# Performance work log

Measured on AMD Instinct MI355X. Metric: run time of the kernel, lower is better.

The kernel has to match this reference:

```python
import jax, jax.numpy as jnp
import numpy as np

B, N, G = 8, 262144, 64
EPS = 1e-6


def _log_transform(x):
    return jnp.sign(x) * jnp.log1p(jnp.abs(x))


def _group_mean_depth(points, valid, groups):
    # points: (B,N,3), valid: (B,N) bool, groups: (B,N) int in [0,G)
    z = points[..., 2]
    w = valid.astype(z.dtype)
    seg = (groups.astype(jnp.int32) + jnp.arange(B, dtype=jnp.int32)[:, None] * G).ravel()
    sums = jax.ops.segment_sum((z * w).ravel(), seg, num_segments=B * G)
    cnts = jax.ops.segment_sum(w.ravel(), seg, num_segments=B * G)
    mean = jnp.where(cnts > 0, sums / jnp.maximum(cnts, 1.0), 1.0)  # empty group -> 1.0 (skipped in torch loop)
    safe = jnp.maximum(jnp.abs(mean), EPS)
    per_point = safe[seg].reshape(z.shape)
    return jnp.where(valid, per_point, 1.0)


def _normalize_points(points, valid, groups):
    md = _group_mean_depth(points, valid, groups)
    return jnp.where(valid[..., None], points, 0.0) / md[..., None]


def _masked_mean(loss, valid):
    vm = valid if loss.ndim == valid.ndim else jnp.broadcast_to(valid[..., None], loss.shape)
    return jnp.where(vm, loss, 0.0).sum() / (vm.sum().astype(loss.dtype) + 1e-6)


def setup_inputs() -> dict:
    key = jax.random.key(0)
    ks = jax.random.split(key, 13)
    f = lambda k, s: jax.random.normal(k, s, dtype=jnp.float32)
    return {
        'pred_points': f(ks[0], (B, N, 3)),
        'target_points': f(ks[1], (B, N, 3)),
        'pred_2d': f(ks[2], (B, N, 2)),
        'target_2d': f(ks[3], (B, N, 2)),
        'pred_vis': f(ks[4], (B, N, 1)),
        'target_vis': jax.random.uniform(ks[5], (B, N), dtype=jnp.float32),
        'pred_disp': f(ks[6], (B, N, 3)),
        'target_disp': f(ks[7], (B, N, 3)),
        'pred_normal': f(ks[8], (B, N, 3)),
        'target_normal': f(ks[9], (B, N, 3)),
        'confidence': f(ks[10], (B, N, 1)),
        'mask': jax.random.randint(ks[11], (B, N), 0, 2, dtype=jnp.int32),
        'groups': jax.random.randint(ks[12], (B, N), 0, G, dtype=jnp.int32),
    }


def reference(pred_points, target_points, pred_2d, target_2d, pred_vis, target_vis,
              pred_disp, target_disp, pred_normal, target_normal, confidence, mask, groups):
    lambda_3d, lambda_raw_3d, lambda_2d = 1.0, 0.0, 0.1
    lambda_vis, lambda_disp, lambda_normal, lambda_conf = 0.1, 0.1, 0.5, 0.2
    valid = mask.astype(bool)

    # L_3D: per-group scale-invariant normalization + log transform + masked L1
    pn = _log_transform(_normalize_points(pred_points, valid, groups))
    tn = _log_transform(_normalize_points(target_points, valid, groups))
    l_3d = _masked_mean(jnp.abs(pn - tn), valid)

    # L_raw3D: raw camera-space L1 (weight 0 by default)
    l_raw3d = _masked_mean(jnp.abs(pred_points - target_points), valid)

    # L_2D
    l_2d = _masked_mean(jnp.abs(pred_2d - target_2d), valid)

    # L_vis: BCE with logits
    x = pred_vis[..., 0]
    bce = jnp.maximum(x, 0.0) - x * target_vis + jnp.log1p(jnp.exp(-jnp.abs(x)))
    l_vis = _masked_mean(bce, valid)

    # L_disp
    l_disp = _masked_mean(jnp.abs(pred_disp - target_disp), valid)

    # L_normal: 1 - cosine similarity of unit-normalized vectors
    def _unit(v):
        n = jnp.linalg.norm(v, axis=-1, keepdims=True)
        return v / jnp.maximum(n, 1e-12)
    cos = (_unit(pred_normal) * _unit(target_normal)).sum(-1)
    l_normal = _masked_mean(1.0 - cos, valid)

    # L_conf: Kendall penalty s = -log(c)
    l_conf = _masked_mean(confidence[..., 0], valid)

    return (lambda_3d * l_3d + lambda_raw_3d * l_raw3d + lambda_2d * l_2d
            + lambda_vis * l_vis + lambda_disp * l_disp
            + lambda_normal * l_normal + lambda_conf * l_conf)
```

## Files before the change

kernel.cpp:

```cpp
#include <hip/hip_runtime.h>
#include <math.h>

#define GG   64
#define NBG  512
#define TOT  2097152
#define PTS  1024
#define NBLK (TOT / PTS)

#define ZP_F   0
#define ZT_F   512
#define CNT_F  1024
#define PAIR_F 1536
#define NV_F   2560
#define PART_F 2816
#define WS_ZERO_BYTES (1536 * 4)

#define LN2   0.6931471805599453f
#define LOG2E 1.4426950408889634f

typedef float vf4 __attribute__((ext_vector_type(4)));
typedef int   vi4 __attribute__((ext_vector_type(4)));

__device__ __forceinline__ float fexp2(float x) { return __builtin_amdgcn_exp2f(x); }
__device__ __forceinline__ float flog2(float x) { return __builtin_amdgcn_logf(x); }
__device__ __forceinline__ float flog1p(float x) { return flog2(1.0f + x) * LN2; }

__device__ __forceinline__ float4 ntl4(const float4* p) {
    vf4 v = __builtin_nontemporal_load((const vf4*)p);
    return make_float4(v.x, v.y, v.z, v.w);
}
__device__ __forceinline__ int4 ntl4i(const int4* p) {
    vi4 v = __builtin_nontemporal_load((const vi4*)p);
    return make_int4(v.x, v.y, v.z, v.w);
}

__device__ __forceinline__ float wredf(float v) {
#pragma unroll
    for (int o = 32; o > 0; o >>= 1) v += __shfl_down(v, o, 64);
    return v;
}

__global__ __launch_bounds__(256) void k_group(const float* __restrict__ pp,
                                               const float* __restrict__ tp,
                                               const int* __restrict__ mask,
                                               const int* __restrict__ grp,
                                               float* __restrict__ ws) {
    __shared__ float4 bufA[768], bufB[768];
    __shared__ float sP[GG], sT[GG], sC[GG];
    const int tid = threadIdx.x;
    if (tid < GG) { sP[tid] = 0.f; sT[tid] = 0.f; sC[tid] = 0.f; }

    const int base = blockIdx.x * PTS;
    const int b = base >> 18;
    const int p0 = base + 4 * tid;

    const float4* gx = (const float4*)(pp + (size_t)base * 3);
    const float4* gy = (const float4*)(tp + (size_t)base * 3);
#pragma unroll
    for (int j = 0; j < 3; j++) {
        bufA[tid + 256 * j] = ntl4(&gx[tid + 256 * j]);
        bufB[tid + 256 * j] = ntl4(&gy[tid + 256 * j]);
    }
    const int4 M  = ntl4i((const int4*)(mask + p0));
    const int4 Gp = ntl4i((const int4*)(grp + p0));
    __syncthreads();

    float4 a0 = bufA[3 * tid], a1 = bufA[3 * tid + 1], a2 = bufA[3 * tid + 2];
    float4 b0 = bufB[3 * tid], b1 = bufB[3 * tid + 1], b2 = bufB[3 * tid + 2];
    if (M.x) { atomicAdd(&sP[Gp.x], a0.z); atomicAdd(&sT[Gp.x], b0.z); atomicAdd(&sC[Gp.x], 1.f); }
    if (M.y) { atomicAdd(&sP[Gp.y], a1.y); atomicAdd(&sT[Gp.y], b1.y); atomicAdd(&sC[Gp.y], 1.f); }
    if (M.z) { atomicAdd(&sP[Gp.z], a2.x); atomicAdd(&sT[Gp.z], b2.x); atomicAdd(&sC[Gp.z], 1.f); }
    if (M.w) { atomicAdd(&sP[Gp.w], a2.w); atomicAdd(&sT[Gp.w], b2.w); atomicAdd(&sC[Gp.w], 1.f); }
    __syncthreads();

    if (tid < GG) {
        float c = sC[tid];
        if (c != 0.0f) {
            int e = b * GG + tid;
            atomicAdd(&ws[ZP_F + e], sP[tid]);
            atomicAdd(&ws[ZT_F + e], sT[tid]);
            atomicAdd(&ws[CNT_F + e], c);
        }
    }
}

__global__ __launch_bounds__(512) void k_groups_final(float* __restrict__ ws) {
    __shared__ float red[NBG];
    int j = threadIdx.x;
    float c  = ws[CNT_F + j];
    float mP = (c > 0.f) ? (ws[ZP_F + j] / fmaxf(c, 1.f)) : 1.0f;
    float mT = (c > 0.f) ? (ws[ZT_F + j] / fmaxf(c, 1.f)) : 1.0f;
    ws[PAIR_F + 2 * j]     = 1.0f / fmaxf(fabsf(mP), 1e-6f);
    ws[PAIR_F + 2 * j + 1] = 1.0f / fmaxf(fabsf(mT), 1e-6f);
    red[j] = c;
    __syncthreads();
    for (int s = 256; s > 0; s >>= 1) {
        if (j < s) red[j] += red[j + s];
        __syncthreads();
    }
    if (j == 0) ws[NV_F] = red[0];
}

__global__ __launch_bounds__(256) void k_loss(const float* __restrict__ pp,
                                              const float* __restrict__ tp,
                                              const float* __restrict__ p2,
                                              const float* __restrict__ t2,
                                              const float* __restrict__ pv,
                                              const float* __restrict__ tv,
                                              const float* __restrict__ pd,
                                              const float* __restrict__ td,
                                              const float* __restrict__ pn,
                                              const float* __restrict__ tn,
                                              const float* __restrict__ cf,
                                              const int* __restrict__ mask,
                                              const int* __restrict__ grp,
                                              float* __restrict__ ws) {
    __shared__ float4 bufA[768], bufB[768];
    const int tid = threadIdx.x;
    const int base = blockIdx.x * PTS;
    const int p0 = base + 4 * tid;
    const int bb6 = (base >> 18) << 6;
    const float* pairs = ws + PAIR_F;

    const int4 M  = ntl4i((const int4*)(mask + p0));
    const int4 Gp = ntl4i((const int4*)(grp + p0));
    const float w[4] = {(float)M.x, (float)M.y, (float)M.z, (float)M.w};
    const int Gs[4] = {Gp.x, Gp.y, Gp.z, Gp.w};
    float iP[4], iT[4];
#pragma unroll
    for (int k = 0; k < 4; k++) {
        float2 pr = *(const float2*)(pairs + 2 * (bb6 | Gs[k]));
        iP[k] = pr.x; iT[k] = pr.y;
    }

    float s3d = 0.f, s2 = 0.f, sv = 0.f, sd = 0.f, sn = 0.f, sc = 0.f;

    {
        float4 Aa = ntl4(((const float4*)(p2 + 2 * (size_t)p0)) + 0);
        float4 Ab = ntl4(((const float4*)(p2 + 2 * (size_t)p0)) + 1);
        float4 Ba = ntl4(((const float4*)(t2 + 2 * (size_t)p0)) + 0);
        float4 Bb = ntl4(((const float4*)(t2 + 2 * (size_t)p0)) + 1);
        s2 = w[0] * (fabsf(Aa.x - Ba.x) + fabsf(Aa.y - Ba.y))
           + w[1] * (fabsf(Aa.z - Ba.z) + fabsf(Aa.w - Ba.w))
           + w[2] * (fabsf(Ab.x - Bb.x) + fabsf(Ab.y - Bb.y))
           + w[3] * (fabsf(Ab.z - Bb.z) + fabsf(Ab.w - Bb.w));
    }
    {
        float4 X  = ntl4((const float4*)(pv + p0));
        float4 Tg = ntl4((const float4*)(tv + p0));
        float4 C  = ntl4((const float4*)(cf + p0));
        const float xs[4] = {X.x, X.y, X.z, X.w};
        const float ts[4] = {Tg.x, Tg.y, Tg.z, Tg.w};
        const float cs[4] = {C.x, C.y, C.z, C.w};
#pragma unroll
        for (int k = 0; k < 4; k++) {
            float x = xs[k];
            float soft = flog2(1.0f + fexp2(-fabsf(x) * LOG2E)) * LN2;
            sv += w[k] * (fmaxf(x, 0.f) - x * ts[k] + soft);
            sc += w[k] * cs[k];
        }
    }

    {
        const float4* gx = (const float4*)(pp + (size_t)base * 3);
        const float4* gy = (const float4*)(tp + (size_t)base * 3);
#pragma unroll
        for (int j = 0; j < 3; j++) {
            bufA[tid + 256 * j] = ntl4(&gx[tid + 256 * j]);
            bufB[tid + 256 * j] = ntl4(&gy[tid + 256 * j]);
        }
        __syncthreads();
        float P[12], T[12];
        *(float4*)&P[0] = bufA[3 * tid]; *(float4*)&P[4] = bufA[3 * tid + 1]; *(float4*)&P[8] = bufA[3 * tid + 2];
        *(float4*)&T[0] = bufB[3 * tid]; *(float4*)&T[4] = bufB[3 * tid + 1]; *(float4*)&T[8] = bufB[3 * tid + 2];
        __syncthreads();
#pragma unroll
        for (int k = 0; k < 4; k++) {
            float acc = 0.f;
#pragma unroll
            for (int c = 0; c < 3; c++) {
                float a = P[3 * k + c] * iP[k];
                float b = T[3 * k + c] * iT[k];
                acc += fabsf(copysignf(flog1p(fabsf(a)), a) - copysignf(flog1p(fabsf(b)), b));
            }
            s3d += w[k] * acc;
        }
    }
    {
        const float4* gx = (const float4*)(pd + (size_t)base * 3);
        const float4* gy = (const float4*)(td + (size_t)base * 3);
#pragma unroll
        for (int j = 0; j < 3; j++) {
            bufA[tid + 256 * j] = ntl4(&gx[tid + 256 * j]);
            bufB[tid + 256 * j] = ntl4(&gy[tid + 256 * j]);
        }
        __syncthreads();
        float P[12], T[12];
        *(float4*)&P[0] = bufA[3 * tid]; *(float4*)&P[4] = bufA[3 * tid + 1]; *(float4*)&P[8] = bufA[3 * tid + 2];
        *(float4*)&T[0] = bufB[3 * tid]; *(float4*)&T[4] = bufB[3 * tid + 1]; *(float4*)&T[8] = bufB[3 * tid + 2];
        __syncthreads();
#pragma unroll
        for (int k = 0; k < 4; k++) {
            float acc = fabsf(P[3 * k] - T[3 * k]) + fabsf(P[3 * k + 1] - T[3 * k + 1])
                      + fabsf(P[3 * k + 2] - T[3 * k + 2]);
            sd += w[k] * acc;
        }
    }
    {
        const float4* gx = (const float4*)(pn + (size_t)base * 3);
        const float4* gy = (const float4*)(tn + (size_t)base * 3);
#pragma unroll
        for (int j = 0; j < 3; j++) {
            bufA[tid + 256 * j] = ntl4(&gx[tid + 256 * j]);
            bufB[tid + 256 * j] = ntl4(&gy[tid + 256 * j]);
        }
        __syncthreads();
        float P[12], T[12];
        *(float4*)&P[0] = bufA[3 * tid]; *(float4*)&P[4] = bufA[3 * tid + 1]; *(float4*)&P[8] = bufA[3 * tid + 2];
        *(float4*)&T[0] = bufB[3 * tid]; *(float4*)&T[4] = bufB[3 * tid + 1]; *(float4*)&T[8] = bufB[3 * tid + 2];
#pragma unroll
        for (int k = 0; k < 4; k++) {
            float ax = P[3 * k], ay = P[3 * k + 1], az = P[3 * k + 2];
            float bx = T[3 * k], by = T[3 * k + 1], bz = T[3 * k + 2];
            float na = fmaf(ax, ax, fmaf(ay, ay, az * az));
            float nb = fmaf(bx, bx, fmaf(by, by, bz * bz));
            float dot = fmaf(ax, bx, fmaf(ay, by, az * bz));
            float r = __frsqrt_rn(fmaxf(na, 1e-24f)) * __frsqrt_rn(fmaxf(nb, 1e-24f));
            sn += w[k] * (1.0f - dot * r);
        }
    }

    __shared__ float sred[4][6];
    float vals[6] = {s3d, s2, sv, sd, sn, sc};
    int wid = threadIdx.x >> 6, lane = threadIdx.x & 63;
#pragma unroll
    for (int k = 0; k < 6; k++) {
        float r = wredf(vals[k]);
        if (lane == 0) sred[wid][k] = r;
    }
    __syncthreads();
    if (threadIdx.x < 6) {
        float tt = sred[0][threadIdx.x] + sred[1][threadIdx.x]
                 + sred[2][threadIdx.x] + sred[3][threadIdx.x];
        ws[PART_F + threadIdx.x * NBLK + blockIdx.x] = tt;
    }
}

__global__ __launch_bounds__(256) void k_final(const float* __restrict__ ws,
                                               float* __restrict__ out) {
    const float* part = ws + PART_F;
    double loc[6] = {0, 0, 0, 0, 0, 0};
    for (int j = threadIdx.x; j < NBLK; j += 256) {
#pragma unroll
        for (int k = 0; k < 6; k++) loc[k] += (double)part[k * NBLK + j];
    }
    __shared__ double dred[4][6];
    int wid = threadIdx.x >> 6, lane = threadIdx.x & 63;
#pragma unroll
    for (int k = 0; k < 6; k++) {
        double v = loc[k];
#pragma unroll
        for (int o = 32; o > 0; o >>= 1) v += __shfl_down(v, o, 64);
        if (lane == 0) dred[wid][k] = v;
    }
    __syncthreads();
    if (threadIdx.x == 0) {
        double a[6];
#pragma unroll
        for (int k = 0; k < 6; k++)
            a[k] = dred[0][k] + dred[1][k] + dred[2][k] + dred[3][k];
        double nv = (double)ws[NV_F];
        double d1 = nv + 1e-6;
        double d3 = 3.0 * nv + 1e-6;
        double l3d   = a[0] / d3;
        double l2d   = a[1] / (2.0 * nv + 1e-6);
        double lvis  = a[2] / d1;
        double ldisp = a[3] / d3;
        double lnorm = a[4] / d1;
        double lconf = a[5] / d1;
        out[0] = (float)(l3d + 0.1 * (l2d + lvis + ldisp) + 0.5 * lnorm + 0.2 * lconf);
    }
}

extern "C" void kernel_launch(void* const* d_in, const int* in_sizes, int n_in,
                              void* d_out, int out_size, void* d_ws, size_t ws_size,
                              hipStream_t stream) {
    const float* pp = (const float*)d_in[0];
    const float* tp = (const float*)d_in[1];
    const float* p2 = (const float*)d_in[2];
    const float* t2 = (const float*)d_in[3];
    const float* pv = (const float*)d_in[4];
    const float* tv = (const float*)d_in[5];
    const float* pd = (const float*)d_in[6];
    const float* td = (const float*)d_in[7];
    const float* pn = (const float*)d_in[8];
    const float* tn = (const float*)d_in[9];
    const float* cf = (const float*)d_in[10];
    const int* mask = (const int*)d_in[11];
    const int* grp  = (const int*)d_in[12];
    float* ws = (float*)d_ws;
    float* out = (float*)d_out;

    (void)hipMemsetAsync(d_ws, 0, WS_ZERO_BYTES, stream);
    k_group<<<NBLK, 256, 0, stream>>>(pp, tp, mask, grp, ws);
    k_groups_final<<<1, NBG, 0, stream>>>(ws);
    k_loss<<<NBLK, 256, 0, stream>>>(pp, tp, p2, t2, pv, tv, pd, td, pn, tn, cf, mask, grp, ws);
    k_final<<<1, 256, 0, stream>>>(ws, out);
}
```

Baseline: 78.95 us.

## Fold group-mean finalize into loss kernel and drop separate launch

Removes the single-block k_groups_final kernel. Each k_loss block now computes inverse mean depths for its own batch's 64 groups into shared memory, and k_final sums the group counts itself to get the valid count. k_group also switches to regular (temporal) loads so pred/target points may stay in cache for the second pass in k_loss. This saves one serialized launch and its latency, at the cost of redundant per-block division work and an extra barrier.

Measured after the change: 79.60 us. Within noise of the previous version (+0.8%).

```diff
diff --git a/kernel.cpp b/kernel.cpp
--- a/kernel.cpp
+++ b/kernel.cpp
@@ -10,9 +10,7 @@
 #define ZP_F   0
 #define ZT_F   512
 #define CNT_F  1024
-#define PAIR_F 1536
-#define NV_F   2560
-#define PART_F 2816
+#define PART_F 1536
 #define WS_ZERO_BYTES (1536 * 4)
 
 #define LN2   0.6931471805599453f
@@ -58,11 +56,11 @@
     const float4* gy = (const float4*)(tp + (size_t)base * 3);
 #pragma unroll
     for (int j = 0; j < 3; j++) {
-        bufA[tid + 256 * j] = ntl4(&gx[tid + 256 * j]);
-        bufB[tid + 256 * j] = ntl4(&gy[tid + 256 * j]);
-    }
-    const int4 M  = ntl4i((const int4*)(mask + p0));
-    const int4 Gp = ntl4i((const int4*)(grp + p0));
+        bufA[tid + 256 * j] = gx[tid + 256 * j];
+        bufB[tid + 256 * j] = gy[tid + 256 * j];
+    }
+    const int4 M  = *(const int4*)(mask + p0);
+    const int4 Gp = *(const int4*)(grp + p0);
     __syncthreads();
 
     float4 a0 = bufA[3 * tid], a1 = bufA[3 * tid + 1], a2 = bufA[3 * tid + 2];
@@ -82,23 +80,6 @@
             atomicAdd(&ws[CNT_F + e], c);
         }
     }
-}
-
-__global__ __launch_bounds__(512) void k_groups_final(float* __restrict__ ws) {
-    __shared__ float red[NBG];
-    int j = threadIdx.x;
-    float c  = ws[CNT_F + j];
-    float mP = (c > 0.f) ? (ws[ZP_F + j] / fmaxf(c, 1.f)) : 1.0f;
-    float mT = (c > 0.f) ? (ws[ZT_F + j] / fmaxf(c, 1.f)) : 1.0f;
-    ws[PAIR_F + 2 * j]     = 1.0f / fmaxf(fabsf(mP), 1e-6f);
-    ws[PAIR_F + 2 * j + 1] = 1.0f / fmaxf(fabsf(mT), 1e-6f);
-    red[j] = c;
-    __syncthreads();
-    for (int s = 256; s > 0; s >>= 1) {
-        if (j < s) red[j] += red[j + s];
-        __syncthreads();
-    }
-    if (j == 0) ws[NV_F] = red[0];
 }
 
 __global__ __launch_bounds__(256) void k_loss(const float* __restrict__ pp,
@@ -116,21 +97,32 @@
                                               const int* __restrict__ grp,
                                               float* __restrict__ ws) {
     __shared__ float4 bufA[768], bufB[768];
+    __shared__ float sPairs[2 * GG];
     const int tid = threadIdx.x;
     const int base = blockIdx.x * PTS;
     const int p0 = base + 4 * tid;
-    const int bb6 = (base >> 18) << 6;
-    const float* pairs = ws + PAIR_F;
+    const int b = base >> 18;
+
+    if (tid < GG) {
+        int e = b * GG + tid;
+        float c = ws[CNT_F + e];
+        float mP = (c > 0.f) ? ws[ZP_F + e] / fmaxf(c, 1.f) : 1.f;
+        float mT = (c > 0.f) ? ws[ZT_F + e] / fmaxf(c, 1.f) : 1.f;
+        sPairs[2 * tid]     = 1.f / fmaxf(fabsf(mP), 1e-6f);
+        sPairs[2 * tid + 1] = 1.f / fmaxf(fabsf(mT), 1e-6f);
+    }
 
     const int4 M  = ntl4i((const int4*)(mask + p0));
     const int4 Gp = ntl4i((const int4*)(grp + p0));
     const float w[4] = {(float)M.x, (float)M.y, (float)M.z, (float)M.w};
     const int Gs[4] = {Gp.x, Gp.y, Gp.z, Gp.w};
+    __syncthreads();
+
     float iP[4], iT[4];
 #pragma unroll
     for (int k = 0; k < 4; k++) {
-        float2 pr = *(const float2*)(pairs + 2 * (bb6 | Gs[k]));
-        iP[k] = pr.x; iT[k] = pr.y;
+        iP[k] = sPairs[2 * Gs[k]];
+        iT[k] = sPairs[2 * Gs[k] + 1];
     }
 
     float s3d = 0.f, s2 = 0.f, sv = 0.f, sd = 0.f, sn = 0.f, sc = 0.f;
@@ -180,8 +172,8 @@
 #pragma unroll
             for (int c = 0; c < 3; c++) {
                 float a = P[3 * k + c] * iP[k];
-                float b = T[3 * k + c] * iT[k];
-                acc += fabsf(copysignf(flog1p(fabsf(a)), a) - copysignf(flog1p(fabsf(b)), b));
+                float bb = T[3 * k + c] * iT[k];
+                acc += fabsf(copysignf(flog1p(fabsf(a)), a) - copysignf(flog1p(fabsf(bb)), bb));
             }
             s3d += w[k] * acc;
         }
@@ -201,9 +193,8 @@
         __syncthreads();
 #pragma unroll
         for (int k = 0; k < 4; k++) {
-            float acc = fabsf(P[3 * k] - T[3 * k]) + fabsf(P[3 * k + 1] - T[3 * k + 1])
-                      + fabsf(P[3 * k + 2] - T[3 * k + 2]);
-            sd += w[k] * acc;
+            sd += w[k] * (fabsf(P[3 * k] - T[3 * k]) + fabsf(P[3 * k + 1] - T[3 * k + 1])
+                        + fabsf(P[3 * k + 2] - T[3 * k + 2]));
         }
     }
     {
@@ -254,7 +245,10 @@
 #pragma unroll
         for (int k = 0; k < 6; k++) loc[k] += (double)part[k * NBLK + j];
     }
+    float nvloc = ws[CNT_F + threadIdx.x] + ws[CNT_F + threadIdx.x + 256];
+
     __shared__ double dred[4][6];
+    __shared__ float nred[4];
     int wid = threadIdx.x >> 6, lane = threadIdx.x & 63;
 #pragma unroll
     for (int k = 0; k < 6; k++) {
@@ -263,13 +257,17 @@
         for (int o = 32; o > 0; o >>= 1) v += __shfl_down(v, o, 64);
         if (lane == 0) dred[wid][k] = v;
     }
+    {
+        float v = wredf(nvloc);
+        if (lane == 0) nred[wid] = v;
+    }
     __syncthreads();
     if (threadIdx.x == 0) {
         double a[6];
 #pragma unroll
         for (int k = 0; k < 6; k++)
             a[k] = dred[0][k] + dred[1][k] + dred[2][k] + dred[3][k];
-        double nv = (double)ws[NV_F];
+        double nv = (double)(nred[0] + nred[1] + nred[2] + nred[3]);
         double d1 = nv + 1e-6;
         double d3 = 3.0 * nv + 1e-6;
         double l3d   = a[0] / d3;
@@ -303,7 +301,6 @@
 
     (void)hipMemsetAsync(d_ws, 0, WS_ZERO_BYTES, stream);
     k_group<<<NBLK, 256, 0, stream>>>(pp, tp, mask, grp, ws);
-    k_groups_final<<<1, NBG, 0, stream>>>(ws);
     k_loss<<<NBLK, 256, 0, stream>>>(pp, tp, p2, t2, pv, tv, pd, td, pn, tn, cf, mask, grp, ws);
     k_final<<<1, 256, 0, stream>>>(ws, out);
 }
```
